# Performance work log

Hardware: AMD Instinct MI355X
Metric: run time of the kernel (lower is better)

## Reference

```python
import jax, jax.numpy as jnp
import numpy as np

B, S, VOCAB = 16384, 50, 100000
EMB = 20
RAW_FEAT = 109            # channel 0 = item id, 108 float features
D = EMB + (RAW_FEAT - 1)  # 128
H = 4 * D                 # 512, pooled concat width
N_BLOCKS = 10
OUT = 20


def setup_inputs() -> dict:
    key = jax.random.key(0)
    ks = jax.random.split(key, 12)
    ids = jax.random.randint(ks[0], (B, S), 0, VOCAB).astype(jnp.float32)
    feats = jax.random.normal(ks[1], (B, S, RAW_FEAT - 1), dtype=jnp.float32)
    inp = jnp.concatenate([ids[:, :, None], feats], axis=2)
    # prefix validity mask with seq_len in [1, S]
    seq_len = jax.random.randint(ks[2], (B,), 1, S + 1)
    mask = (jnp.arange(S)[None, :] < seq_len[:, None]).astype(jnp.int64)
    embed = jax.random.normal(ks[3], (VOCAB, EMB), dtype=jnp.float32) * 0.02
    s1 = 1.0 / np.sqrt(H)
    s2 = 1.0 / np.sqrt(4 * H)
    W1 = jax.random.uniform(ks[4], (N_BLOCKS, H, 4 * H), minval=-s1, maxval=s1)
    b1 = jax.random.uniform(ks[5], (N_BLOCKS, 4 * H), minval=-s1, maxval=s1)
    W2 = jax.random.uniform(ks[6], (N_BLOCKS, 4 * H, H), minval=-s2, maxval=s2)
    b2 = jax.random.uniform(ks[7], (N_BLOCKS, H), minval=-s2, maxval=s2)
    Wf = jax.random.uniform(ks[8], (H, OUT), minval=-s1, maxval=s1)
    bf = jax.random.uniform(ks[9], (OUT,), minval=-s1, maxval=s1)
    return {"input": inp, "mask": mask, "embed": embed, "W1": W1, "b1": b1,
            "W2": W2, "b2": b2, "Wf": Wf, "bf": bf}


def reference(input, mask, embed, W1, b1, W2, b2, Wf, bf):
    ids = input[:, :, 0].astype(jnp.int32)
    x = jnp.concatenate([embed[ids], input[:, :, 1:]], axis=2)  # [B,S,D]
    next_item = x[:, -1, :]                                      # [B,D]
    seq_len = jnp.sum(mask, axis=1)                              # [B]
    valid = (jnp.arange(x.shape[1])[None, :] < seq_len[:, None])[:, :, None]
    # masked mean / max / min over the valid prefix (vectorized)
    denom = seq_len[:, None].astype(x.dtype)
    avg = jnp.sum(jnp.where(valid, x, 0.0), axis=1) / denom
    mx = jnp.clip(jnp.max(jnp.where(valid, x, -jnp.inf), axis=1), 1e-9, 1e9)
    mn = jnp.clip(jnp.min(jnp.where(valid, x, jnp.inf), axis=1), 1e-9, 1e9)
    h = jnp.concatenate([avg, mx, mn, next_item], axis=1)        # [B,4D]
    for i in range(W1.shape[0]):  # 10 residual widen blocks (dropout=eval identity)
        t = jax.nn.relu(h @ W1[i] + b1[i])
        t = jax.nn.relu(t @ W2[i] + b2[i])
        h = h + t
    return h @ Wf + bf
```

## Files before the change

kernel.cpp:

```cpp
#include <hip/hip_runtime.h>
#include <stdint.h>

typedef unsigned short ushort_t;
typedef __attribute__((ext_vector_type(8))) __bf16 bf16x8;
typedef __attribute__((ext_vector_type(4))) float f32x4;

#define B_SZ 16384
#define SEQ 50
#define RAWF 109
#define EMB 20
#define DFEAT 128
#define H 512
#define H4 2048
#define NBLK 10
#define OUTD 20

__device__ __forceinline__ ushort_t f2bf(float f) {
    union { float f; uint32_t u; } v; v.f = f;
    uint32_t r = (v.u + 0x7fffu + ((v.u >> 16) & 1u)) >> 16;
    return (ushort_t)r;
}

__global__ __launch_bounds__(256)
void transpose_bf16_kernel(const float* __restrict__ src, ushort_t* __restrict__ dst,
                           int K, int N) {
    __shared__ float tile[64][65];
    const int i = blockIdx.z;
    const float* s = src + (size_t)i * K * N;
    ushort_t* d = dst + (size_t)i * K * N;
    const int t = threadIdx.x;
    const int rr = t >> 4;
    const int cc = t & 15;
    const int k0 = blockIdx.y * 64, n0 = blockIdx.x * 64;
#pragma unroll
    for (int r = 0; r < 4; ++r) {
        const int kr = rr + r * 16;
        const float4 v = *(const float4*)(s + (size_t)(k0 + kr) * N + n0 + cc * 4);
        tile[kr][cc * 4 + 0] = v.x;
        tile[kr][cc * 4 + 1] = v.y;
        tile[kr][cc * 4 + 2] = v.z;
        tile[kr][cc * 4 + 3] = v.w;
    }
    __syncthreads();
#pragma unroll
    for (int r = 0; r < 4; ++r) {
        const int nr = rr + r * 16;
        ushort4 o;
        o.x = f2bf(tile[cc * 4 + 0][nr]);
        o.y = f2bf(tile[cc * 4 + 1][nr]);
        o.z = f2bf(tile[cc * 4 + 2][nr]);
        o.w = f2bf(tile[cc * 4 + 3][nr]);
        *(ushort4*)(d + (size_t)(n0 + nr) * K + k0 + cc * 4) = o;
    }
}

__global__ __launch_bounds__(256)
void len_kernel(const int* __restrict__ mask, int* __restrict__ len) {
    const int wid = (blockIdx.x * 256 + threadIdx.x) >> 6;
    const int lane = threadIdx.x & 63;
    if (wid >= B_SZ) return;
    int c = (lane < SEQ) ? mask[(size_t)wid * SEQ + lane] : 0;
#pragma unroll
    for (int off = 32; off > 0; off >>= 1) c += __shfl_down(c, off);
    c = __shfl(c, 0);
    if (lane == 0) len[wid] = c;
}

__global__ __launch_bounds__(128)
void rawfeat_kernel(const float* __restrict__ inp, const int* __restrict__ len,
                    float* __restrict__ hf, ushort_t* __restrict__ hb,
                    int* __restrict__ ids) {
    const int b = blockIdx.x;
    const int jj = threadIdx.x;
    const float* src = inp + (size_t)b * SEQ * RAWF;
    const int L = len[b];
    const bool active = jj < RAWF;
    float sum = 0.f, mx = -3.0e38f, mn = 3.0e38f, nxt = 0.f;
#pragma unroll 10
    for (int s = 0; s < SEQ; ++s) {
        float v = active ? src[s * RAWF + jj] : 0.f;
        if (s < L) { sum += v; mx = fmaxf(mx, v); mn = fminf(mn, v); }
        if (s == SEQ - 1) nxt = v;
        if (jj == 0) ids[(size_t)b * SEQ + s] = (int)v;
    }
    if (jj >= 1 && jj < RAWF) {
        const int j = 19 + jj;
        const float avg = sum / (float)L;
        mx = fminf(fmaxf(mx, 1e-9f), 1e9f);
        mn = fminf(fmaxf(mn, 1e-9f), 1e9f);
        const size_t base = (size_t)b * H;
        hf[base + j] = avg;             hb[base + j] = f2bf(avg);
        hf[base + DFEAT + j] = mx;      hb[base + DFEAT + j] = f2bf(mx);
        hf[base + 2 * DFEAT + j] = mn;  hb[base + 2 * DFEAT + j] = f2bf(mn);
        hf[base + 3 * DFEAT + j] = nxt; hb[base + 3 * DFEAT + j] = f2bf(nxt);
    }
}

__global__ __launch_bounds__(256)
void embfeat_kernel(const int* __restrict__ ids, const int* __restrict__ len,
                    const float* __restrict__ embed,
                    float* __restrict__ hf, ushort_t* __restrict__ hb) {
    const int x = threadIdx.x & 31;
    const int row = (blockIdx.x * 256 + threadIdx.x) >> 5;
    if (row >= B_SZ) return;
    const int L = len[row];
    const int* idrow = ids + (size_t)row * SEQ;
    const bool act = x < EMB;
    float sum = 0.f, mx = -3.0e38f, mn = 3.0e38f, nxt = 0.f;
#pragma unroll 10
    for (int s = 0; s < SEQ; ++s) {
        const int id = idrow[s];
        const float v = act ? embed[(size_t)id * EMB + x] : 0.f;
        if (s < L) { sum += v; mx = fmaxf(mx, v); mn = fminf(mn, v); }
        if (s == SEQ - 1) nxt = v;
    }
    if (act) {
        const float avg = sum / (float)L;
        mx = fminf(fmaxf(mx, 1e-9f), 1e9f);
        mn = fminf(fmaxf(mn, 1e-9f), 1e9f);
        const size_t base = (size_t)row * H;
        hf[base + x] = avg;             hb[base + x] = f2bf(avg);
        hf[base + DFEAT + x] = mx;      hb[base + DFEAT + x] = f2bf(mx);
        hf[base + 2 * DFEAT + x] = mn;  hb[base + 2 * DFEAT + x] = f2bf(mn);
        hf[base + 3 * DFEAT + x] = nxt; hb[base + 3 * DFEAT + x] = f2bf(nxt);
    }
}

template <int MODE>
__global__ __launch_bounds__(256, 3)
void gemm_kernel(const ushort_t* __restrict__ A, const ushort_t* __restrict__ Bt,
                 const float* __restrict__ bias,
                 ushort_t* __restrict__ outBf,
                 float* __restrict__ hf, ushort_t* __restrict__ hb,
                 int M, int N, int K) {
    __shared__ alignas(16) ushort_t lA[128 * 64];
    __shared__ alignas(16) ushort_t lB[128 * 64];
    const int tid = threadIdx.x;
    const int lane = tid & 63;
    const int w = tid >> 6;
    const int wm = w >> 1, wn = w & 1;

    const int gx = N >> 7;
    const int nwg = (M >> 7) * gx;
    const int cpx = nwg >> 3;
    const int bid = blockIdx.x;
    const int wg = (bid & 7) * cpx + (bid >> 3);
    const int ntile = wg % gx, mtile = wg / gx;

    const ushort_t* Abase = A + (size_t)mtile * 128 * K;
    const ushort_t* Bbase = Bt + (size_t)ntile * 128 * K;

    f32x4 acc[4][4];
#pragma unroll
    for (int a = 0; a < 4; ++a)
#pragma unroll
        for (int b = 0; b < 4; ++b) acc[a][b] = (f32x4)(0.f);

    const int l3 = lane >> 3;
    const int cl = (lane & 7) ^ l3;
    const int frow = lane & 15;
    const int k16b = lane >> 4;

    const int nkt = K >> 6;
    for (int kt = 0; kt < nkt; ++kt) {
#pragma unroll
        for (int it = 0; it < 4; ++it) {
            const int row = w * 32 + it * 8 + l3;
            const ushort_t* ga = Abase + (size_t)row * K + kt * 64 + cl * 8;
            const ushort_t* gb = Bbase + (size_t)row * K + kt * 64 + cl * 8;
            __builtin_amdgcn_global_load_lds(
                (const __attribute__((address_space(1))) void*)ga,
                (__attribute__((address_space(3))) void*)(lA + (w * 32 + it * 8) * 64),
                16, 0, 0);
            __builtin_amdgcn_global_load_lds(
                (const __attribute__((address_space(1))) void*)gb,
                (__attribute__((address_space(3))) void*)(lB + (w * 32 + it * 8) * 64),
                16, 0, 0);
        }
        asm volatile("s_waitcnt vmcnt(0)" ::: "memory");
        __syncthreads();

        bf16x8 af[4][2], bfg[4][2];
#pragma unroll
        for (int mf = 0; mf < 4; ++mf)
#pragma unroll
            for (int ks = 0; ks < 2; ++ks) {
                const int row = wm * 64 + mf * 16 + frow;
                const int c = (ks * 4 + k16b) ^ (row & 7);
                af[mf][ks] = *(const bf16x8*)(lA + row * 64 + c * 8);
            }
#pragma unroll
        for (int nf = 0; nf < 4; ++nf)
#pragma unroll
            for (int ks = 0; ks < 2; ++ks) {
                const int row = wn * 64 + nf * 16 + frow;
                const int c = (ks * 4 + k16b) ^ (row & 7);
                bfg[nf][ks] = *(const bf16x8*)(lB + row * 64 + c * 8);
            }
#pragma unroll
        for (int mf = 0; mf < 4; ++mf)
#pragma unroll
            for (int nf = 0; nf < 4; ++nf)
#pragma unroll
                for (int ks = 0; ks < 2; ++ks)
                    acc[mf][nf] = __builtin_amdgcn_mfma_f32_16x16x32_bf16(
                        af[mf][ks], bfg[nf][ks], acc[mf][nf], 0, 0, 0);
        __syncthreads();
    }

#pragma unroll
    for (int mf = 0; mf < 4; ++mf)
#pragma unroll
        for (int nf = 0; nf < 4; ++nf) {
            const int row0 = mtile * 128 + wm * 64 + mf * 16 + (lane >> 4) * 4;
            const int col = ntile * 128 + wn * 64 + nf * 16 + (lane & 15);
            const float bcol = bias[col];
#pragma unroll
            for (int jj = 0; jj < 4; ++jj) {
                float v = acc[mf][nf][jj] + bcol;
                v = v > 0.f ? v : 0.f;
                const size_t idx = (size_t)(row0 + jj) * N + col;
                if (MODE == 0) {
                    outBf[idx] = f2bf(v);
                } else {
                    float nh = hf[idx] + v;
                    hf[idx] = nh;
                    hb[idx] = f2bf(nh);
                }
            }
        }
}

__global__ __launch_bounds__(256)
void final_kernel(const float* __restrict__ hf, const float* __restrict__ Wf,
                  const float* __restrict__ bfv, float* __restrict__ out) {
    const int gid = blockIdx.x * 256 + threadIdx.x;
    if (gid >= B_SZ * OUTD) return;
    const int b = gid / OUTD, o = gid % OUTD;
    const float* hrow = hf + (size_t)b * H;
    float acc = bfv[o];
    for (int k = 0; k < H; ++k) acc += hrow[k] * Wf[k * OUTD + o];
    out[gid] = acc;
}

extern "C" void kernel_launch(void* const* d_in, const int* in_sizes, int n_in,
                              void* d_out, int out_size, void* d_ws, size_t ws_size,
                              hipStream_t stream) {
    const float* inp   = (const float*)d_in[0];
    const int*   mask  = (const int*)d_in[1];
    const float* embed = (const float*)d_in[2];
    const float* W1    = (const float*)d_in[3];
    const float* b1    = (const float*)d_in[4];
    const float* W2    = (const float*)d_in[5];
    const float* b2    = (const float*)d_in[6];
    const float* Wf    = (const float*)d_in[7];
    const float* bfv   = (const float*)d_in[8];
    float* out = (float*)d_out;

    char* ws = (char*)d_ws;
    ushort_t* W1t = (ushort_t*)ws;
    ushort_t* W2t = W1t + (size_t)NBLK * H4 * H;
    float*    hf  = (float*)(W2t + (size_t)NBLK * H * H4);
    ushort_t* hb  = (ushort_t*)(hf + (size_t)B_SZ * H);
    ushort_t* T   = hb + (size_t)B_SZ * H;
    int* ids = (int*)T;
    int* lenb = ids + (size_t)B_SZ * SEQ;

    transpose_bf16_kernel<<<dim3(H4 / 64, H / 64, NBLK), 256, 0, stream>>>(W1, W1t, H, H4);
    transpose_bf16_kernel<<<dim3(H / 64, H4 / 64, NBLK), 256, 0, stream>>>(W2, W2t, H4, H);

    len_kernel<<<(B_SZ * 64 + 255) / 256, 256, 0, stream>>>(mask, lenb);
    rawfeat_kernel<<<B_SZ, 128, 0, stream>>>(inp, lenb, hf, hb, ids);
    embfeat_kernel<<<(B_SZ * 32 + 255) / 256, 256, 0, stream>>>(ids, lenb, embed, hf, hb);

    for (int i = 0; i < NBLK; ++i) {
        gemm_kernel<0><<<(B_SZ / 128) * (H4 / 128), 256, 0, stream>>>(
            hb, W1t + (size_t)i * H4 * H, b1 + (size_t)i * H4, T, nullptr, nullptr,
            B_SZ, H4, H);
        gemm_kernel<1><<<(B_SZ / 128) * (H / 128), 256, 0, stream>>>(
            T, W2t + (size_t)i * H * H4, b2 + (size_t)i * H, nullptr, hf, hb,
            B_SZ, H, H4);
    }

    final_kernel<<<(B_SZ * OUTD + 255) / 256, 256, 0, stream>>>(hf, Wf, bfv, out);
}
```

Baseline: 1.306 ms.

## Replace first GEMM with 256x256 double-buffered 8-phase pipelined kernel

The W1 GEMM (K=512, N=2048) moves to a new 512-thread kernel with 256x256 tiles and double-buffered LDS. Each K-step is split into four quadrant phases that interleave direct global-to-LDS loads for future tiles with MFMA work, using barriers and raised wave priority. The aim is to hide load latency and raise data reuse compared with the old single-buffered 128x128 kernel, which waited for every load before computing. The cost is 128KB of LDS per block and much more complex synchronization. The second GEMM is unchanged apart from dropping the template.

```diff
diff --git a/kernel.cpp b/kernel.cpp
--- a/kernel.cpp
+++ b/kernel.cpp
@@ -19,6 +19,12 @@
     union { float f; uint32_t u; } v; v.f = f;
     uint32_t r = (v.u + 0x7fffu + ((v.u >> 16) & 1u)) >> 16;
     return (ushort_t)r;
+}
+
+__device__ __forceinline__ void glds16(const ushort_t* src, ushort_t* dst) {
+    __builtin_amdgcn_global_load_lds(
+        (const __attribute__((address_space(1))) void*)src,
+        (__attribute__((address_space(3))) void*)dst, 16, 0, 0);
 }
 
 __global__ __launch_bounds__(256)
@@ -126,13 +132,168 @@
     }
 }
 
-template <int MODE>
+__global__ __launch_bounds__(512, 2)
+void gemm1_8phase(const ushort_t* __restrict__ A, const ushort_t* __restrict__ Bt,
+                  const float* __restrict__ bias, ushort_t* __restrict__ outBf,
+                  int M, int N, int K) {
+    __shared__ alignas(16) ushort_t lAb[2][256 * 64];
+    __shared__ alignas(16) ushort_t lBb[2][256 * 64];
+    const int tid = threadIdx.x;
+    const int lane = tid & 63;
+    const int w = tid >> 6;
+    const int wm = w >> 2;
+    const int wn = w & 3;
+    const int frow = lane & 15;
+    const int k16 = lane >> 4;
+
+    const int gx = N >> 8;
+    const int nwg = (M >> 8) * gx;
+    const int cpx = nwg >> 3;
+    const int bid = blockIdx.x;
+    const int wg = (bid & 7) * cpx + (bid >> 3);
+    const int ntile = wg % gx, mtile = wg / gx;
+
+    const ushort_t* Abase = A + (size_t)mtile * 256 * K;
+    const ushort_t* Bbase = Bt + (size_t)ntile * 256 * K;
+
+    const int l3 = lane >> 3;
+    const int csrc = (lane & 7) ^ l3;
+    const int hr0 = w * 16 + l3, hr1 = hr0 + 8;
+    const ushort_t* pA00 = Abase + (size_t)(((hr0 >> 6) << 7) + (hr0 & 63)) * K + csrc * 8;
+    const ushort_t* pA01 = Abase + (size_t)(((hr1 >> 6) << 7) + (hr1 & 63)) * K + csrc * 8;
+    const ushort_t* pA10 = Abase + (size_t)(((hr0 >> 6) << 7) + 64 + (hr0 & 63)) * K + csrc * 8;
+    const ushort_t* pA11 = Abase + (size_t)(((hr1 >> 6) << 7) + 64 + (hr1 & 63)) * K + csrc * 8;
+    const ushort_t* pB00 = Bbase + (size_t)(((hr0 >> 5) << 6) + (hr0 & 31)) * K + csrc * 8;
+    const ushort_t* pB01 = Bbase + (size_t)(((hr1 >> 5) << 6) + (hr1 & 31)) * K + csrc * 8;
+    const ushort_t* pB10 = Bbase + (size_t)(((hr0 >> 5) << 6) + 32 + (hr0 & 31)) * K + csrc * 8;
+    const ushort_t* pB11 = Bbase + (size_t)(((hr1 >> 5) << 6) + 32 + (hr1 & 31)) * K + csrc * 8;
+    const int d0 = (w * 16) * 64, d1 = (w * 16 + 8) * 64;
+
+    f32x4 acc00[4][2], acc01[4][2], acc10[4][2], acc11[4][2];
+#pragma unroll
+    for (int mf = 0; mf < 4; ++mf)
+#pragma unroll
+        for (int nf = 0; nf < 2; ++nf) {
+            acc00[mf][nf] = (f32x4)(0.f); acc01[mf][nf] = (f32x4)(0.f);
+            acc10[mf][nf] = (f32x4)(0.f); acc11[mf][nf] = (f32x4)(0.f);
+        }
+
+    auto stage2 = [&](ushort_t* base, int halfofs, const ushort_t* s0,
+                      const ushort_t* s1, int kt) {
+        const size_t ko = (size_t)kt * 64;
+        glds16(s0 + ko, base + halfofs + d0);
+        glds16(s1 + ko, base + halfofs + d1);
+    };
+    auto readA = [&](const ushort_t* la, int mh, bf16x8 (&af)[4][2]) {
+#pragma unroll
+        for (int mf = 0; mf < 4; ++mf)
+#pragma unroll
+            for (int ks = 0; ks < 2; ++ks) {
+                const int row = mh * 128 + wm * 64 + mf * 16 + frow;
+                const int c = (ks * 4 + k16) ^ (frow & 7);
+                af[mf][ks] = *(const bf16x8*)(la + row * 64 + c * 8);
+            }
+    };
+    auto readB = [&](const ushort_t* lb, int nh, bf16x8 (&bq)[2][2]) {
+#pragma unroll
+        for (int nf = 0; nf < 2; ++nf)
+#pragma unroll
+            for (int ks = 0; ks < 2; ++ks) {
+                const int row = nh * 128 + wn * 32 + nf * 16 + frow;
+                const int c = (ks * 4 + k16) ^ (frow & 7);
+                bq[nf][ks] = *(const bf16x8*)(lb + row * 64 + c * 8);
+            }
+    };
+    auto mfmaQ = [&](bf16x8 (&af)[4][2], bf16x8 (&bq)[2][2], f32x4 (&ac)[4][2]) {
+        __builtin_amdgcn_s_setprio(1);
+#pragma unroll
+        for (int mf = 0; mf < 4; ++mf)
+#pragma unroll
+            for (int nf = 0; nf < 2; ++nf)
+#pragma unroll
+                for (int ks = 0; ks < 2; ++ks)
+                    ac[mf][nf] = __builtin_amdgcn_mfma_f32_16x16x32_bf16(
+                        af[mf][ks], bq[nf][ks], ac[mf][nf], 0, 0, 0);
+        __builtin_amdgcn_s_setprio(0);
+    };
+
+    const int nkt = K >> 6;
+    bf16x8 af[4][2], b0q[2][2], b1q[2][2];
+
+    stage2(lAb[0], 0,    pA00, pA01, 0);
+    stage2(lBb[0], 0,    pB00, pB01, 0);
+    stage2(lAb[0], 8192, pA10, pA11, 0);
+    stage2(lBb[0], 8192, pB10, pB11, 0);
+    stage2(lAb[1], 0,    pA00, pA01, 1);
+    stage2(lBb[1], 0,    pB00, pB01, 1);
+    stage2(lAb[1], 8192, pA10, pA11, 1);
+    asm volatile("s_waitcnt vmcnt(6)" ::: "memory");
+    __builtin_amdgcn_s_barrier();
+
+    for (int t = 0; t < nkt; ++t) {
+        ushort_t* la = lAb[t & 1];
+        ushort_t* lb = lBb[t & 1];
+        ushort_t* lbN = lBb[(t + 1) & 1];
+        const bool s1 = (t + 1) < nkt;
+        const bool s2 = (t + 2) < nkt;
+        readA(la, 0, af);
+        readB(lb, 0, b0q);
+        if (s1) stage2(lbN, 8192, pB10, pB11, t + 1);
+        __builtin_amdgcn_s_barrier();
+        asm volatile("s_waitcnt lgkmcnt(0)" ::: "memory");
+        __builtin_amdgcn_sched_barrier(0);
+        mfmaQ(af, b0q, acc00);
+        __builtin_amdgcn_s_barrier();
+        readB(lb, 1, b1q);
+        if (s2) stage2(la, 0, pA00, pA01, t + 2);
+        __builtin_amdgcn_s_barrier();
+        asm volatile("s_waitcnt lgkmcnt(0)" ::: "memory");
+        __builtin_amdgcn_sched_barrier(0);
+        mfmaQ(af, b1q, acc01);
+        __builtin_amdgcn_s_barrier();
+        readA(la, 1, af);
+        if (s2) stage2(lb, 0, pB00, pB01, t + 2);
+        __builtin_amdgcn_s_barrier();
+        asm volatile("s_waitcnt lgkmcnt(0)" ::: "memory");
+        __builtin_amdgcn_sched_barrier(0);
+        mfmaQ(af, b0q, acc10);
+        __builtin_amdgcn_s_barrier();
+        if (s2) {
+            stage2(la, 8192, pA10, pA11, t + 2);
+            asm volatile("s_waitcnt vmcnt(6)" ::: "memory");
+        } else {
+            asm volatile("s_waitcnt vmcnt(0)" ::: "memory");
+        }
+        __builtin_amdgcn_s_barrier();
+        __builtin_amdgcn_sched_barrier(0);
+        mfmaQ(af, b1q, acc11);
+        __builtin_amdgcn_s_barrier();
+    }
+
+    auto epi = [&](f32x4 (&ac)[4][2], int mh, int nh) {
+#pragma unroll
+        for (int mf = 0; mf < 4; ++mf)
+#pragma unroll
+            for (int nf = 0; nf < 2; ++nf) {
+                const int row0 = mtile * 256 + wm * 128 + mh * 64 + mf * 16 + (lane >> 4) * 4;
+                const int col = ntile * 256 + wn * 64 + nh * 32 + nf * 16 + (lane & 15);
+                const float bc = bias[col];
+#pragma unroll
+                for (int jj = 0; jj < 4; ++jj) {
+                    float v = ac[mf][nf][jj] + bc;
+                    v = v > 0.f ? v : 0.f;
+                    outBf[(size_t)(row0 + jj) * N + col] = f2bf(v);
+                }
+            }
+    };
+    epi(acc00, 0, 0); epi(acc01, 0, 1); epi(acc10, 1, 0); epi(acc11, 1, 1);
+}
+
 __global__ __launch_bounds__(256, 3)
-void gemm_kernel(const ushort_t* __restrict__ A, const ushort_t* __restrict__ Bt,
-                 const float* __restrict__ bias,
-                 ushort_t* __restrict__ outBf,
-                 float* __restrict__ hf, ushort_t* __restrict__ hb,
-                 int M, int N, int K) {
+void gemm2_kernel(const ushort_t* __restrict__ A, const ushort_t* __restrict__ Bt,
+                  const float* __restrict__ bias,
+                  float* __restrict__ hf, ushort_t* __restrict__ hb,
+                  int M, int N, int K) {
     __shared__ alignas(16) ushort_t lA[128 * 64];
     __shared__ alignas(16) ushort_t lB[128 * 64];
     const int tid = threadIdx.x;
@@ -168,14 +329,8 @@
             const int row = w * 32 + it * 8 + l3;
             const ushort_t* ga = Abase + (size_t)row * K + kt * 64 + cl * 8;
             const ushort_t* gb = Bbase + (size_t)row * K + kt * 64 + cl * 8;
-            __builtin_amdgcn_global_load_lds(
-                (const __attribute__((address_space(1))) void*)ga,
-                (__attribute__((address_space(3))) void*)(lA + (w * 32 + it * 8) * 64),
-                16, 0, 0);
-            __builtin_amdgcn_global_load_lds(
-                (const __attribute__((address_space(1))) void*)gb,
-                (__attribute__((address_space(3))) void*)(lB + (w * 32 + it * 8) * 64),
-                16, 0, 0);
+            glds16(ga, lA + (w * 32 + it * 8) * 64);
+            glds16(gb, lB + (w * 32 + it * 8) * 64);
         }
         asm volatile("s_waitcnt vmcnt(0)" ::: "memory");
         __syncthreads();
@@ -220,13 +375,9 @@
                 float v = acc[mf][nf][jj] + bcol;
                 v = v > 0.f ? v : 0.f;
                 const size_t idx = (size_t)(row0 + jj) * N + col;
-                if (MODE == 0) {
-                    outBf[idx] = f2bf(v);
-                } else {
-                    float nh = hf[idx] + v;
-                    hf[idx] = nh;
-                    hb[idx] = f2bf(nh);
-                }
+                float nh = hf[idx] + v;
+                hf[idx] = nh;
+                hb[idx] = f2bf(nh);
             }
         }
 }
@@ -274,11 +425,10 @@
     embfeat_kernel<<<(B_SZ * 32 + 255) / 256, 256, 0, stream>>>(ids, lenb, embed, hf, hb);
 
     for (int i = 0; i < NBLK; ++i) {
-        gemm_kernel<0><<<(B_SZ / 128) * (H4 / 128), 256, 0, stream>>>(
-            hb, W1t + (size_t)i * H4 * H, b1 + (size_t)i * H4, T, nullptr, nullptr,
-            B_SZ, H4, H);
-        gemm_kernel<1><<<(B_SZ / 128) * (H / 128), 256, 0, stream>>>(
-            T, W2t + (size_t)i * H * H4, b2 + (size_t)i * H, nullptr, hf, hb,
+        gemm1_8phase<<<(B_SZ / 256) * (H4 / 256), 512, 0, stream>>>(
+            hb, W1t + (size_t)i * H4 * H, b1 + (size_t)i * H4, T, B_SZ, H4, H);
+        gemm2_kernel<<<(B_SZ / 128) * (H / 128), 256, 0, stream>>>(
+            T, W2t + (size_t)i * H * H4, b2 + (size_t)i * H, hf, hb,
             B_SZ, H, H4);
     }
 
```

Result: slower. 1.397 ms (+7.0%).
